# Kernel tuning notes

Hardware: AMD Instinct MI355X
Metric: run time of the kernel (lower is better)

The kernel has to match this reference:

```python
import jax, jax.numpy as jnp
import numpy as np

N_HEADS = 4
DIM_HEAD = 32
SCALE = DIM_HEAD ** -0.5
EPS = 1e-5


def setup_inputs() -> dict:
    key = jax.random.key(0)
    ks = jax.random.split(key, 5)
    b, dim, l, h, w = 8, 128, 32, 32, 32
    hidden = N_HEADS * DIM_HEAD  # 128
    return {
        "x": jax.random.normal(ks[0], (b, dim, l, h, w), dtype=jnp.float32),
        "w_qkv": jax.random.normal(ks[1], (3 * hidden, dim), dtype=jnp.float32) * 0.05,
        "w_out": jax.random.normal(ks[2], (dim, hidden), dtype=jnp.float32) * 0.05,
        "b_out": jax.random.normal(ks[3], (dim,), dtype=jnp.float32) * 0.05,
        "gn_gamma": jnp.ones((dim,), dtype=jnp.float32),
        "gn_beta": jnp.zeros((dim,), dtype=jnp.float32),
    }


def reference(x, w_qkv, w_out, b_out, gn_gamma, gn_beta):
    b, dim, l, h_sp, w_sp = x.shape
    n = l * h_sp * w_sp
    hidden = N_HEADS * DIM_HEAD
    xf = x.reshape(b, dim, n)  # flatten spatial -> tokens
    # 1x1 conv == channel matmul: [3*hidden, dim] x [b, dim, n]
    qkv = jnp.einsum('oc,bcn->bon', w_qkv, xf)
    qkv = qkv.reshape(b, 3, N_HEADS, DIM_HEAD, n)
    q, k, v = qkv[:, 0], qkv[:, 1], qkv[:, 2]  # each [b, H, d, n]
    q = jax.nn.softmax(q, axis=2) * SCALE      # softmax over feature dim d
    k = jax.nn.softmax(k, axis=-1)             # softmax over tokens n
    c = jnp.einsum('bhdn,bhen->bhde', k, v)    # [b, H, d, e] tiny context
    out = jnp.einsum('bhde,bhdn->bhen', c, q)  # [b, H, e, n]
    out = out.reshape(b, hidden, n)
    # to_out 1x1 conv + bias
    y = jnp.einsum('oc,bcn->bon', w_out, out) + b_out[None, :, None]
    # GroupNorm(1, dim): normalize over (C, spatial) per sample
    mean = jnp.mean(y, axis=(1, 2), keepdims=True)
    var = jnp.var(y, axis=(1, 2), keepdims=True)
    y = (y - mean) * jax.lax.rsqrt(var + EPS)
    y = y * gn_gamma[None, :, None] + gn_beta[None, :, None]
    return y.reshape(b, dim, l, h_sp, w_sp)
```

## Files before the change

### kernel.cpp

```cpp
#include <hip/hip_runtime.h>

#define BATCH 8
#define DIMC 128
#define NTOT 32768
#define HEADS 4
#define DHEAD 32
#define SCALE_Q 0.17677669529663687f
#define GRIDX 64
#define TILES 8

typedef _Float16 half8  __attribute__((ext_vector_type(8)));
typedef _Float16 half4v __attribute__((ext_vector_type(4)));
typedef float    f32x4  __attribute__((ext_vector_type(4)));

#define WS_WQKV 0
#define WS_S    98304
#define WS_Z    229376
#define WS_ST   233472
#define WS_GOFF 0
#define WS_NEED 299072


__global__ void k0_prep(const float* __restrict__ wqkv, char* __restrict__ ws) {
    int i = blockIdx.x * 256 + threadIdx.x;
    _Float16* Wb = (_Float16*)(ws + WS_WQKV);
    float* S  = (float*)(ws + WS_S);
    float* Z  = (float*)(ws + WS_Z);
    float* St = (float*)(ws + WS_ST);
    if (i < 49152) Wb[i] = (_Float16)wqkv[i];
    int j = i - 49152;
    if (j >= 0 && j < 32768) S[j] = 0.f;
    int k = j - 32768;
    if (k >= 0 && k < 1024) Z[k] = 0.f;
    int m = k - 1024;
    if (m >= 0 && m < 16) St[m] = 0.f;
}

__global__ __launch_bounds__(256, 1) void k1_kv(const float* __restrict__ x,
                                                const _Float16* __restrict__ Wb,
                                                float* __restrict__ S,
                                                float* __restrict__ Z,
                                                char* __restrict__ ybase) {
    __shared__ _Float16 Xb[64][136];
    __shared__ _Float16 KB[128][64];
    __shared__ _Float16 VB[128][64];
    __shared__ _Float16 EQT[64][136];
    const int t = threadIdx.x;
    const int lane = t & 63, w = t >> 6, g = lane >> 4, l15 = lane & 15;
    const int b = blockIdx.y;

    half8 wa[2][4];
    half8 af[4][4];
#pragma unroll
    for (int mi = 0; mi < 2; ++mi)
#pragma unroll
        for (int kc = 0; kc < 4; ++kc)
            wa[mi][kc] = *(const half8*)(Wb + (size_t)((w * 2 + mi) * 16 + l15) * 128 + kc * 32 + 8 * g);
#pragma unroll
    for (int mt = 0; mt < 4; ++mt)
#pragma unroll
        for (int kc = 0; kc < 4; ++kc)
            af[mt][kc] = *(const half8*)(Wb + (size_t)(128 + (w * 4 + mt) * 16 + l15) * 128 + kc * 32 + 8 * g);

    half8 vone;
#pragma unroll
    for (int i = 0; i < 8; ++i) vone[i] = (_Float16)1.0f;

    f32x4 sacc[2][2];
#pragma unroll
    for (int dm = 0; dm < 2; ++dm)
#pragma unroll
        for (int en = 0; en < 2; ++en) sacc[dm][en] = (f32x4){0.f, 0.f, 0.f, 0.f};
    f32x4 zacc[2];
    zacc[0] = (f32x4){0.f, 0.f, 0.f, 0.f};
    zacc[1] = (f32x4){0.f, 0.f, 0.f, 0.f};

    const int j4 = t & 15, c0 = t >> 4;
    const int sxw = (j4 & 7) << 3;

    float4 xr[8];
#pragma unroll
    for (int cc = 0; cc < 8; ++cc)
        xr[cc] = *(const float4*)(x + ((size_t)b * DIMC + c0 + 16 * cc) * NTOT + blockIdx.x * 64 + 4 * j4);
#pragma unroll
    for (int cc = 0; cc < 8; ++cc) {
        const int c = c0 + 16 * cc;
        Xb[4 * j4 + 0][c ^ sxw] = (_Float16)xr[cc].x;
        Xb[4 * j4 + 1][c ^ sxw] = (_Float16)xr[cc].y;
        Xb[4 * j4 + 2][c ^ sxw] = (_Float16)xr[cc].z;
        Xb[4 * j4 + 3][c ^ sxw] = (_Float16)xr[cc].w;
    }

    for (int it = 0; it < TILES; ++it) {
        const int j0 = (blockIdx.x + GRIDX * it) * 64;
        __syncthreads();
        half8 bf[4][4];
#pragma unroll
        for (int nt = 0; nt < 4; ++nt) {
            const int sb = ((4 * nt + (l15 >> 2)) & 7) << 3;
#pragma unroll
            for (int kc = 0; kc < 4; ++kc)
                bf[nt][kc] = *(const half8*)(&Xb[nt * 16 + l15][(kc * 32 + 8 * g) ^ sb]);
        }
        {
            f32x4 eacc[2][4];
#pragma unroll
            for (int mi = 0; mi < 2; ++mi)
#pragma unroll
                for (int nt = 0; nt < 4; ++nt) eacc[mi][nt] = (f32x4){0.f, 0.f, 0.f, 0.f};
#pragma unroll
            for (int mi = 0; mi < 2; ++mi)
#pragma unroll
                for (int kc = 0; kc < 4; ++kc)
#pragma unroll
                    for (int nt = 0; nt < 4; ++nt)
                        eacc[mi][nt] = __builtin_amdgcn_mfma_f32_16x16x32_f16(wa[mi][kc], bf[nt][kc], eacc[mi][nt], 0, 0, 0);
            float ps[4] = {0.f, 0.f, 0.f, 0.f};
#pragma unroll
            for (int mi = 0; mi < 2; ++mi)
#pragma unroll
                for (int nt = 0; nt < 4; ++nt)
#pragma unroll
                    for (int r = 0; r < 4; ++r) {
                        const float e = __expf(eacc[mi][nt][r]);
                        ps[nt] += e;
                        eacc[mi][nt][r] = e;
                    }
            float scn[4];
#pragma unroll
            for (int nt = 0; nt < 4; ++nt) {
                ps[nt] += __shfl_xor(ps[nt], 16);
                ps[nt] += __shfl_xor(ps[nt], 32);
                scn[nt] = SCALE_Q / ps[nt];
            }
#pragma unroll
            for (int mi = 0; mi < 2; ++mi)
#pragma unroll
                for (int nt = 0; nt < 4; ++nt) {
                    half4v p;
#pragma unroll
                    for (int r = 0; r < 4; ++r) p[r] = (_Float16)(eacc[mi][nt][r] * scn[nt]);
                    *(half4v*)(&EQT[nt * 16 + l15][(w * 2 + mi) * 16 + g * 4]) = p;
                }
        }
        if (it < TILES - 1) {
            const int j0n = (blockIdx.x + GRIDX * (it + 1)) * 64;
#pragma unroll
            for (int cc = 0; cc < 8; ++cc)
                xr[cc] = *(const float4*)(x + ((size_t)b * DIMC + c0 + 16 * cc) * NTOT + j0n + 4 * j4);
        }
#pragma unroll
        for (int mt = 0; mt < 4; ++mt) {
            f32x4 a0 = (f32x4){0.f,0.f,0.f,0.f}, a1 = a0, a2 = a0, a3 = a0;
#pragma unroll
            for (int kc = 0; kc < 4; ++kc) {
                a0 = __builtin_amdgcn_mfma_f32_16x16x32_f16(bf[0][kc], af[mt][kc], a0, 0, 0, 0);
                a1 = __builtin_amdgcn_mfma_f32_16x16x32_f16(bf[1][kc], af[mt][kc], a1, 0, 0, 0);
                a2 = __builtin_amdgcn_mfma_f32_16x16x32_f16(bf[2][kc], af[mt][kc], a2, 0, 0, 0);
                a3 = __builtin_amdgcn_mfma_f32_16x16x32_f16(bf[3][kc], af[mt][kc], a3, 0, 0, 0);
            }
            const int row16 = (w * 4 + mt) * 16;
            const int sk = ((mt * 4 + (l15 >> 2)) & 7) << 3;
            if (row16 < 128) {
#pragma unroll
                for (int jt = 0; jt < 4; ++jt) {
                    const f32x4 a = (jt == 0) ? a0 : (jt == 1) ? a1 : (jt == 2) ? a2 : a3;
                    half4v p;
#pragma unroll
                    for (int r = 0; r < 4; ++r) p[r] = (_Float16)__expf(a[r]);
                    *(half4v*)(&KB[row16 + l15][(jt * 16 + g * 4) ^ sk]) = p;
                }
            } else {
#pragma unroll
                for (int jt = 0; jt < 4; ++jt) {
                    const f32x4 a = (jt == 0) ? a0 : (jt == 1) ? a1 : (jt == 2) ? a2 : a3;
                    half4v p;
#pragma unroll
                    for (int r = 0; r < 4; ++r) p[r] = (_Float16)a[r];
                    *(half4v*)(&VB[row16 - 128 + l15][(jt * 16 + g * 4) ^ sk]) = p;
                }
            }
        }
        __syncthreads();
        if (it < TILES - 1) {
#pragma unroll
            for (int cc = 0; cc < 8; ++cc) {
                const int c = c0 + 16 * cc;
                Xb[4 * j4 + 0][c ^ sxw] = (_Float16)xr[cc].x;
                Xb[4 * j4 + 1][c ^ sxw] = (_Float16)xr[cc].y;
                Xb[4 * j4 + 2][c ^ sxw] = (_Float16)xr[cc].z;
                Xb[4 * j4 + 3][c ^ sxw] = (_Float16)xr[cc].w;
            }
        }
#pragma unroll
        for (int dm = 0; dm < 2; ++dm) {
            const int sr = ((4 * dm + (l15 >> 2)) & 7) << 3;
            half8 ka0 = *(const half8*)(&KB[w * 32 + dm * 16 + l15][(8 * g) ^ sr]);
            half8 ka1 = *(const half8*)(&KB[w * 32 + dm * 16 + l15][(32 + 8 * g) ^ sr]);
            zacc[dm] = __builtin_amdgcn_mfma_f32_16x16x32_f16(ka0, vone, zacc[dm], 0, 0, 0);
            zacc[dm] = __builtin_amdgcn_mfma_f32_16x16x32_f16(ka1, vone, zacc[dm], 0, 0, 0);
#pragma unroll
            for (int en = 0; en < 2; ++en) {
                const int se = ((4 * en + (l15 >> 2)) & 7) << 3;
                half8 vb0 = *(const half8*)(&VB[w * 32 + en * 16 + l15][(8 * g) ^ se]);
                half8 vb1 = *(const half8*)(&VB[w * 32 + en * 16 + l15][(32 + 8 * g) ^ se]);
                sacc[dm][en] = __builtin_amdgcn_mfma_f32_16x16x32_f16(ka0, vb0, sacc[dm][en], 0, 0, 0);
                sacc[dm][en] = __builtin_amdgcn_mfma_f32_16x16x32_f16(ka1, vb1, sacc[dm][en], 0, 0, 0);
            }
        }
        {
            char* tb = ybase + (size_t)(b * DIMC + (j0 >> 8)) * 131072 + (size_t)(j0 & 255) * 256;
#pragma unroll
            for (int p = 0; p < 4; ++p) {
                const int idx = p * 256 + t, jl = idx >> 4, d0 = (idx & 15) * 8;
                half8 v = *(const half8*)(&EQT[jl][d0]);
                *(half8*)(tb + (size_t)jl * 256 + d0 * 2) = v;
            }
        }
    }
    if (l15 == 0) {
#pragma unroll
        for (int dm = 0; dm < 2; ++dm)
#pragma unroll
            for (int r = 0; r < 4; ++r)
                atomicAdd(&Z[(b * HEADS + w) * DHEAD + dm * 16 + g * 4 + r], zacc[dm][r]);
    }
#pragma unroll
    for (int dm = 0; dm < 2; ++dm)
#pragma unroll
        for (int en = 0; en < 2; ++en)
#pragma unroll
            for (int r = 0; r < 4; ++r)
                atomicAdd(&S[((size_t)(b * HEADS + w) * DHEAD + dm * 16 + g * 4 + r) * DHEAD + en * 16 + l15],
                          sacc[dm][en][r]);
}

__global__ __launch_bounds__(256) void k2_g(const float* __restrict__ S, const float* __restrict__ Z,
                                            const float* __restrict__ wout, _Float16* __restrict__ G) {
    __shared__ float Sd[32][33];
    const int h = blockIdx.x, b = blockIdx.y;
    const int t = threadIdx.x;
    const float* Sb = S + (size_t)(b * HEADS + h) * 1024;
    const float* Zb = Z + (size_t)(b * HEADS + h) * 32;
    for (int i = t; i < 1024; i += 256) {
        int d = i >> 5;
        Sd[d][i & 31] = Sb[i] / Zb[d];
    }
    __syncthreads();
    const int o = t & 127, dh = (t >> 7) * 16;
    float wrow[32];
#pragma unroll
    for (int e = 0; e < 32; ++e) wrow[e] = wout[o * 128 + h * 32 + e];
    _Float16* Gb = G + (size_t)b * 16384;
#pragma unroll
    for (int dd = 0; dd < 16; ++dd) {
        const int d = dh + dd;
        float acc = 0.f;
#pragma unroll
        for (int e = 0; e < 32; ++e) acc = fmaf(wrow[e], Sd[d][e], acc);
        Gb[o * 128 + h * 32 + d] = (_Float16)acc;
    }
}

__global__ __launch_bounds__(256, 2) void k3_main(const _Float16* __restrict__ G,
                                                  const float* __restrict__ b_out,
                                                  char* __restrict__ ybase,
                                                  float* __restrict__ St) {
    __shared__ _Float16 EB[64][136];
    __shared__ float red[8];
    const int t = threadIdx.x;
    const int lane = t & 63, w = t >> 6, g = lane >> 4, l15 = lane & 15;
    const int b = blockIdx.y;

    half8 ga[2][4];
    float bo[2][4];
    const _Float16* Gb = G + (size_t)b * 16384;
#pragma unroll
    for (int mi = 0; mi < 2; ++mi) {
        const int o = (w * 2 + mi) * 16 + l15;
#pragma unroll
        for (int kc = 0; kc < 4; ++kc)
            ga[mi][kc] = *(const half8*)(Gb + (size_t)o * 128 + kc * 32 + 8 * g);
#pragma unroll
        for (int r = 0; r < 4; ++r) bo[mi][r] = b_out[(w * 2 + mi) * 16 + g * 4 + r];
    }

    float ssum = 0.f, ssq = 0.f;
    half8 er[4];

    {
        const int jb = blockIdx.x * 64;
        const char* tb = ybase + (size_t)(b * DIMC + (jb >> 8)) * 131072 + (size_t)(jb & 255) * 256;
#pragma unroll
        for (int p = 0; p < 4; ++p) {
            const int idx = p * 256 + t, jl = idx >> 4, d0 = (idx & 15) * 8;
            er[p] = *(const half8*)(tb + (size_t)jl * 256 + d0 * 2);
        }
#pragma unroll
        for (int p = 0; p < 4; ++p) {
            const int idx = p * 256 + t, jl = idx >> 4, d0 = (idx & 15) * 8;
            *(half8*)(&EB[jl][d0 ^ (((jl >> 2) & 7) << 3)]) = er[p];
        }
    }
    __syncthreads();

    for (int it = 0; it < TILES; ++it) {
        const int j0 = (blockIdx.x + GRIDX * it) * 64;
        if (it < TILES - 1) {
            const int jn = (blockIdx.x + GRIDX * (it + 1)) * 64;
            const char* tb = ybase + (size_t)(b * DIMC + (jn >> 8)) * 131072 + (size_t)(jn & 255) * 256;
#pragma unroll
            for (int p = 0; p < 4; ++p) {
                const int idx = p * 256 + t, jl = idx >> 4, d0 = (idx & 15) * 8;
                er[p] = *(const half8*)(tb + (size_t)jl * 256 + d0 * 2);
            }
        }
        {
            half8 bf[4][4];
#pragma unroll
            for (int nt = 0; nt < 4; ++nt) {
                const int sb = ((4 * nt + (l15 >> 2)) & 7) << 3;
#pragma unroll
                for (int kc = 0; kc < 4; ++kc)
                    bf[nt][kc] = *(const half8*)(&EB[nt * 16 + l15][(kc * 32 + 8 * g) ^ sb]);
            }
#pragma unroll
            for (int mi = 0; mi < 2; ++mi) {
                const int o0 = (w * 2 + mi) * 16 + g * 4;
                f32x4 acc[4];
#pragma unroll
                for (int nt = 0; nt < 4; ++nt) acc[nt] = (f32x4){0.f, 0.f, 0.f, 0.f};
#pragma unroll
                for (int kc = 0; kc < 4; ++kc)
#pragma unroll
                    for (int nt = 0; nt < 4; ++nt)
                        acc[nt] = __builtin_amdgcn_mfma_f32_16x16x32_f16(ga[mi][kc], bf[nt][kc], acc[nt], 0, 0, 0);
#pragma unroll
                for (int r = 0; r < 4; ++r) {
                    _Float16* yrow = (_Float16*)(ybase + (size_t)(b * DIMC + o0 + r) * 131072 + 65536);
#pragma unroll
                    for (int nt = 0; nt < 4; ++nt) {
                        const float yv = acc[nt][r] + bo[mi][r];
                        ssum += yv;
                        ssq += yv * yv;
                        yrow[j0 + nt * 16 + l15] = (_Float16)yv;
                    }
                }
            }
        }
        __syncthreads();
        if (it < TILES - 1) {
#pragma unroll
            for (int p = 0; p < 4; ++p) {
                const int idx = p * 256 + t, jl = idx >> 4, d0 = (idx & 15) * 8;
                *(half8*)(&EB[jl][d0 ^ (((jl >> 2) & 7) << 3)]) = er[p];
            }
        }
        __syncthreads();
    }
#pragma unroll
    for (int m = 32; m; m >>= 1) { ssum += __shfl_xor(ssum, m); ssq += __shfl_xor(ssq, m); }
    if (lane == 0) { red[w] = ssum; red[4 + w] = ssq; }
    __syncthreads();
    if (t == 0) {
        atomicAdd(&St[b * 2 + 0], red[0] + red[1] + red[2] + red[3]);
        atomicAdd(&St[b * 2 + 1], red[4] + red[5] + red[6] + red[7]);
    }
}

__global__ __launch_bounds__(256) void k4_norm(float* __restrict__ out, const float* __restrict__ St,
                                               const float* __restrict__ gamma,
                                               const float* __restrict__ beta) {
    const int o = blockIdx.x;
    const int b = blockIdx.y;
    const int t = threadIdx.x;
    const size_t row = (size_t)b * DIMC + o;
    const float n = (float)DIMC * (float)NTOT;
    const float mean = St[b * 2] / n;
    const float var = St[b * 2 + 1] / n - mean * mean;
    const float rs = rsqrtf(var + 1e-5f);
    const float ga = gamma[o] * rs;
    const float be = beta[o];
    const half8* yh = (const half8*)((const char*)out + row * 131072 + 65536);
    half8 hbuf[16];
#pragma unroll
    for (int i = 0; i < 16; ++i) hbuf[i] = yh[i * 256 + t];
    __syncthreads();
    float4* orow = (float4*)(out + row * NTOT);
#pragma unroll
    for (int i = 0; i < 16; ++i) {
        const int e4 = (i * 256 + t) * 2;
        float4 v0, v1;
        v0.x = ((float)hbuf[i][0] - mean) * ga + be;
        v0.y = ((float)hbuf[i][1] - mean) * ga + be;
        v0.z = ((float)hbuf[i][2] - mean) * ga + be;
        v0.w = ((float)hbuf[i][3] - mean) * ga + be;
        v1.x = ((float)hbuf[i][4] - mean) * ga + be;
        v1.y = ((float)hbuf[i][5] - mean) * ga + be;
        v1.z = ((float)hbuf[i][6] - mean) * ga + be;
        v1.w = ((float)hbuf[i][7] - mean) * ga + be;
        orow[e4] = v0;
        orow[e4 + 1] = v1;
    }
}

extern "C" void kernel_launch(void* const* d_in, const int* in_sizes, int n_in,
                              void* d_out, int out_size, void* d_ws, size_t ws_size,
                              hipStream_t stream) {
    const float* x     = (const float*)d_in[0];
    const float* wqkv  = (const float*)d_in[1];
    const float* wout  = (const float*)d_in[2];
    const float* b_out = (const float*)d_in[3];
    const float* gamma = (const float*)d_in[4];
    const float* beta  = (const float*)d_in[5];
    if (ws_size < WS_NEED) return;
    char* ws = (char*)d_ws;
    _Float16* Wb = (_Float16*)(ws + WS_WQKV);
    float* S  = (float*)(ws + WS_S);
    float* Z  = (float*)(ws + WS_Z);
    float* St = (float*)(ws + WS_ST);
    _Float16* G = (_Float16*)(ws + WS_GOFF);

    k0_prep<<<325, 256, 0, stream>>>(wqkv, ws);
    k1_kv<<<dim3(GRIDX, 8), 256, 0, stream>>>(x, Wb, S, Z, (char*)d_out);
    k2_g<<<dim3(HEADS, 8), 256, 0, stream>>>(S, Z, wout, G);
    k3_main<<<dim3(GRIDX, 8), 256, 0, stream>>>(G, b_out, (char*)d_out, St);
    k4_norm<<<dim3(128, 8), 256, 0, stream>>>((float*)d_out, St, gamma, beta);
}
```

Measured before the change: 156.9 us.

## Recompute q softmax in main kernel from x instead of storing it

The feature-dim q softmax moves out of the KV kernel and into the main output kernel, which now recomputes q from x on the fly. This removes the fp16 q write in the first pass and its read back in the main pass. In exchange, x is read twice in fp32 and the main kernel does extra MFMA and exp work. The main kernel's occupancy hint also drops from 2 to 1 block per CU. The G matrix now lives in spare space of the output buffer so that the fp16 W_qkv copy survives for the main kernel.

```diff
diff --git a/kernel.cpp b/kernel.cpp
--- a/kernel.cpp
+++ b/kernel.cpp
@@ -17,8 +17,7 @@
 #define WS_S    98304
 #define WS_Z    229376
 #define WS_ST   233472
-#define WS_GOFF 0
-#define WS_NEED 299072
+#define WS_NEED 233600
 
 
 __global__ void k0_prep(const float* __restrict__ wqkv, char* __restrict__ ws) {
@@ -39,23 +38,15 @@
 __global__ __launch_bounds__(256, 1) void k1_kv(const float* __restrict__ x,
                                                 const _Float16* __restrict__ Wb,
                                                 float* __restrict__ S,
-                                                float* __restrict__ Z,
-                                                char* __restrict__ ybase) {
+                                                float* __restrict__ Z) {
     __shared__ _Float16 Xb[64][136];
     __shared__ _Float16 KB[128][64];
     __shared__ _Float16 VB[128][64];
-    __shared__ _Float16 EQT[64][136];
     const int t = threadIdx.x;
     const int lane = t & 63, w = t >> 6, g = lane >> 4, l15 = lane & 15;
     const int b = blockIdx.y;
 
-    half8 wa[2][4];
     half8 af[4][4];
-#pragma unroll
-    for (int mi = 0; mi < 2; ++mi)
-#pragma unroll
-        for (int kc = 0; kc < 4; ++kc)
-            wa[mi][kc] = *(const half8*)(Wb + (size_t)((w * 2 + mi) * 16 + l15) * 128 + kc * 32 + 8 * g);
 #pragma unroll
     for (int mt = 0; mt < 4; ++mt)
 #pragma unroll
@@ -92,7 +83,6 @@
     }
 
     for (int it = 0; it < TILES; ++it) {
-        const int j0 = (blockIdx.x + GRIDX * it) * 64;
         __syncthreads();
         half8 bf[4][4];
 #pragma unroll
@@ -101,47 +91,6 @@
 #pragma unroll
             for (int kc = 0; kc < 4; ++kc)
                 bf[nt][kc] = *(const half8*)(&Xb[nt * 16 + l15][(kc * 32 + 8 * g) ^ sb]);
-        }
-        {
-            f32x4 eacc[2][4];
-#pragma unroll
-            for (int mi = 0; mi < 2; ++mi)
-#pragma unroll
-                for (int nt = 0; nt < 4; ++nt) eacc[mi][nt] = (f32x4){0.f, 0.f, 0.f, 0.f};
-#pragma unroll
-            for (int mi = 0; mi < 2; ++mi)
-#pragma unroll
-                for (int kc = 0; kc < 4; ++kc)
-#pragma unroll
-                    for (int nt = 0; nt < 4; ++nt)
-                        eacc[mi][nt] = __builtin_amdgcn_mfma_f32_16x16x32_f16(wa[mi][kc], bf[nt][kc], eacc[mi][nt], 0, 0, 0);
-            float ps[4] = {0.f, 0.f, 0.f, 0.f};
-#pragma unroll
-            for (int mi = 0; mi < 2; ++mi)
-#pragma unroll
-                for (int nt = 0; nt < 4; ++nt)
-#pragma unroll
-                    for (int r = 0; r < 4; ++r) {
-                        const float e = __expf(eacc[mi][nt][r]);
-                        ps[nt] += e;
-                        eacc[mi][nt][r] = e;
-                    }
-            float scn[4];
-#pragma unroll
-            for (int nt = 0; nt < 4; ++nt) {
-                ps[nt] += __shfl_xor(ps[nt], 16);
-                ps[nt] += __shfl_xor(ps[nt], 32);
-                scn[nt] = SCALE_Q / ps[nt];
-            }
-#pragma unroll
-            for (int mi = 0; mi < 2; ++mi)
-#pragma unroll
-                for (int nt = 0; nt < 4; ++nt) {
-                    half4v p;
-#pragma unroll
-                    for (int r = 0; r < 4; ++r) p[r] = (_Float16)(eacc[mi][nt][r] * scn[nt]);
-                    *(half4v*)(&EQT[nt * 16 + l15][(w * 2 + mi) * 16 + g * 4]) = p;
-                }
         }
         if (it < TILES - 1) {
             const int j0n = (blockIdx.x + GRIDX * (it + 1)) * 64;
@@ -208,15 +157,6 @@
                 sacc[dm][en] = __builtin_amdgcn_mfma_f32_16x16x32_f16(ka1, vb1, sacc[dm][en], 0, 0, 0);
             }
         }
-        {
-            char* tb = ybase + (size_t)(b * DIMC + (j0 >> 8)) * 131072 + (size_t)(j0 & 255) * 256;
-#pragma unroll
-            for (int p = 0; p < 4; ++p) {
-                const int idx = p * 256 + t, jl = idx >> 4, d0 = (idx & 15) * 8;
-                half8 v = *(const half8*)(&EQT[jl][d0]);
-                *(half8*)(tb + (size_t)jl * 256 + d0 * 2) = v;
-            }
-        }
     }
     if (l15 == 0) {
 #pragma unroll
@@ -236,7 +176,7 @@
 }
 
 __global__ __launch_bounds__(256) void k2_g(const float* __restrict__ S, const float* __restrict__ Z,
-                                            const float* __restrict__ wout, _Float16* __restrict__ G) {
+                                            const float* __restrict__ wout, char* __restrict__ ybase) {
     __shared__ float Sd[32][33];
     const int h = blockIdx.x, b = blockIdx.y;
     const int t = threadIdx.x;
@@ -251,7 +191,7 @@
     float wrow[32];
 #pragma unroll
     for (int e = 0; e < 32; ++e) wrow[e] = wout[o * 128 + h * 32 + e];
-    _Float16* Gb = G + (size_t)b * 16384;
+    _Float16* Gb = (_Float16*)(ybase + (size_t)(b * 16) * 131072);
 #pragma unroll
     for (int dd = 0; dd < 16; ++dd) {
         const int d = dh + dd;
@@ -262,58 +202,59 @@
     }
 }
 
-__global__ __launch_bounds__(256, 2) void k3_main(const _Float16* __restrict__ G,
+__global__ __launch_bounds__(256, 1) void k3_main(const float* __restrict__ x,
+                                                  const _Float16* __restrict__ Wb,
                                                   const float* __restrict__ b_out,
                                                   char* __restrict__ ybase,
                                                   float* __restrict__ St) {
-    __shared__ _Float16 EB[64][136];
+    __shared__ _Float16 Xb[64][136];
+    __shared__ _Float16 qT[64][136];
     __shared__ float red[8];
     const int t = threadIdx.x;
     const int lane = t & 63, w = t >> 6, g = lane >> 4, l15 = lane & 15;
     const int b = blockIdx.y;
-
+    const int j4 = t & 15, c0 = t >> 4;
+    const int sxw = (j4 & 7) << 3;
+
+    half8 wa[2][4];
     half8 ga[2][4];
     float bo[2][4];
-    const _Float16* Gb = G + (size_t)b * 16384;
+    const _Float16* Gb = (const _Float16*)(ybase + (size_t)(b * 16) * 131072);
 #pragma unroll
     for (int mi = 0; mi < 2; ++mi) {
         const int o = (w * 2 + mi) * 16 + l15;
 #pragma unroll
-        for (int kc = 0; kc < 4; ++kc)
+        for (int kc = 0; kc < 4; ++kc) {
+            wa[mi][kc] = *(const half8*)(Wb + (size_t)o * 128 + kc * 32 + 8 * g);
             ga[mi][kc] = *(const half8*)(Gb + (size_t)o * 128 + kc * 32 + 8 * g);
+        }
 #pragma unroll
         for (int r = 0; r < 4; ++r) bo[mi][r] = b_out[(w * 2 + mi) * 16 + g * 4 + r];
     }
 
     float ssum = 0.f, ssq = 0.f;
-    half8 er[4];
-
-    {
-        const int jb = blockIdx.x * 64;
-        const char* tb = ybase + (size_t)(b * DIMC + (jb >> 8)) * 131072 + (size_t)(jb & 255) * 256;
-#pragma unroll
-        for (int p = 0; p < 4; ++p) {
-            const int idx = p * 256 + t, jl = idx >> 4, d0 = (idx & 15) * 8;
-            er[p] = *(const half8*)(tb + (size_t)jl * 256 + d0 * 2);
-        }
-#pragma unroll
-        for (int p = 0; p < 4; ++p) {
-            const int idx = p * 256 + t, jl = idx >> 4, d0 = (idx & 15) * 8;
-            *(half8*)(&EB[jl][d0 ^ (((jl >> 2) & 7) << 3)]) = er[p];
-        }
+
+    float4 xr[8];
+#pragma unroll
+    for (int cc = 0; cc < 8; ++cc)
+        xr[cc] = *(const float4*)(x + ((size_t)b * DIMC + c0 + 16 * cc) * NTOT + blockIdx.x * 64 + 4 * j4);
+#pragma unroll
+    for (int cc = 0; cc < 8; ++cc) {
+        const int c = c0 + 16 * cc;
+        Xb[4 * j4 + 0][c ^ sxw] = (_Float16)xr[cc].x;
+        Xb[4 * j4 + 1][c ^ sxw] = (_Float16)xr[cc].y;
+        Xb[4 * j4 + 2][c ^ sxw] = (_Float16)xr[cc].z;
+        Xb[4 * j4 + 3][c ^ sxw] = (_Float16)xr[cc].w;
     }
     __syncthreads();
 
     for (int it = 0; it < TILES; ++it) {
         const int j0 = (blockIdx.x + GRIDX * it) * 64;
         if (it < TILES - 1) {
-            const int jn = (blockIdx.x + GRIDX * (it + 1)) * 64;
-            const char* tb = ybase + (size_t)(b * DIMC + (jn >> 8)) * 131072 + (size_t)(jn & 255) * 256;
-#pragma unroll
-            for (int p = 0; p < 4; ++p) {
-                const int idx = p * 256 + t, jl = idx >> 4, d0 = (idx & 15) * 8;
-                er[p] = *(const half8*)(tb + (size_t)jl * 256 + d0 * 2);
-            }
+            const int j0n = (blockIdx.x + GRIDX * (it + 1)) * 64;
+#pragma unroll
+            for (int cc = 0; cc < 8; ++cc)
+                xr[cc] = *(const float4*)(x + ((size_t)b * DIMC + c0 + 16 * cc) * NTOT + j0n + 4 * j4);
         }
         {
             half8 bf[4][4];
@@ -322,8 +263,66 @@
                 const int sb = ((4 * nt + (l15 >> 2)) & 7) << 3;
 #pragma unroll
                 for (int kc = 0; kc < 4; ++kc)
-                    bf[nt][kc] = *(const half8*)(&EB[nt * 16 + l15][(kc * 32 + 8 * g) ^ sb]);
-            }
+                    bf[nt][kc] = *(const half8*)(&Xb[nt * 16 + l15][(kc * 32 + 8 * g) ^ sb]);
+            }
+            f32x4 eacc[2][4];
+#pragma unroll
+            for (int mi = 0; mi < 2; ++mi)
+#pragma unroll
+                for (int nt = 0; nt < 4; ++nt) eacc[mi][nt] = (f32x4){0.f, 0.f, 0.f, 0.f};
+#pragma unroll
+            for (int mi = 0; mi < 2; ++mi)
+#pragma unroll
+                for (int kc = 0; kc < 4; ++kc)
+#pragma unroll
+                    for (int nt = 0; nt < 4; ++nt)
+                        eacc[mi][nt] = __builtin_amdgcn_mfma_f32_16x16x32_f16(wa[mi][kc], bf[nt][kc], eacc[mi][nt], 0, 0, 0);
+            float ps[4] = {0.f, 0.f, 0.f, 0.f};
+#pragma unroll
+            for (int mi = 0; mi < 2; ++mi)
+#pragma unroll
+                for (int nt = 0; nt < 4; ++nt)
+#pragma unroll
+                    for (int r = 0; r < 4; ++r) {
+                        const float e = __expf(eacc[mi][nt][r]);
+                        ps[nt] += e;
+                        eacc[mi][nt][r] = e;
+                    }
+            float scn[4];
+#pragma unroll
+            for (int nt = 0; nt < 4; ++nt) {
+                ps[nt] += __shfl_xor(ps[nt], 16);
+                ps[nt] += __shfl_xor(ps[nt], 32);
+                scn[nt] = SCALE_Q / ps[nt];
+            }
+#pragma unroll
+            for (int mi = 0; mi < 2; ++mi)
+#pragma unroll
+                for (int nt = 0; nt < 4; ++nt) {
+                    half4v p;
+#pragma unroll
+                    for (int r = 0; r < 4; ++r) p[r] = (_Float16)(eacc[mi][nt][r] * scn[nt]);
+                    *(half4v*)(&qT[nt * 16 + l15][((w * 2 + mi) * 16 + g * 4)]) = p;
+                }
+        }
+        __syncthreads();
+        if (it < TILES - 1) {
+#pragma unroll
+            for (int cc = 0; cc < 8; ++cc) {
+                const int c = c0 + 16 * cc;
+                Xb[4 * j4 + 0][c ^ sxw] = (_Float16)xr[cc].x;
+                Xb[4 * j4 + 1][c ^ sxw] = (_Float16)xr[cc].y;
+                Xb[4 * j4 + 2][c ^ sxw] = (_Float16)xr[cc].z;
+                Xb[4 * j4 + 3][c ^ sxw] = (_Float16)xr[cc].w;
+            }
+        }
+        {
+            half8 bf[4][4];
+#pragma unroll
+            for (int nt = 0; nt < 4; ++nt)
+#pragma unroll
+                for (int kc = 0; kc < 4; ++kc)
+                    bf[nt][kc] = *(const half8*)(&qT[nt * 16 + l15][kc * 32 + 8 * g]);
 #pragma unroll
             for (int mi = 0; mi < 2; ++mi) {
                 const int o0 = (w * 2 + mi) * 16 + g * 4;
@@ -346,14 +345,6 @@
                         yrow[j0 + nt * 16 + l15] = (_Float16)yv;
                     }
                 }
-            }
-        }
-        __syncthreads();
-        if (it < TILES - 1) {
-#pragma unroll
-            for (int p = 0; p < 4; ++p) {
-                const int idx = p * 256 + t, jl = idx >> 4, d0 = (idx & 15) * 8;
-                *(half8*)(&EB[jl][d0 ^ (((jl >> 2) & 7) << 3)]) = er[p];
             }
         }
         __syncthreads();
@@ -419,11 +410,10 @@
     float* S  = (float*)(ws + WS_S);
     float* Z  = (float*)(ws + WS_Z);
     float* St = (float*)(ws + WS_ST);
-    _Float16* G = (_Float16*)(ws + WS_GOFF);
 
     k0_prep<<<325, 256, 0, stream>>>(wqkv, ws);
-    k1_kv<<<dim3(GRIDX, 8), 256, 0, stream>>>(x, Wb, S, Z, (char*)d_out);
-    k2_g<<<dim3(HEADS, 8), 256, 0, stream>>>(S, Z, wout, G);
-    k3_main<<<dim3(GRIDX, 8), 256, 0, stream>>>(G, b_out, (char*)d_out, St);
+    k1_kv<<<dim3(GRIDX, 8), 256, 0, stream>>>(x, Wb, S, Z);
+    k2_g<<<dim3(HEADS, 8), 256, 0, stream>>>(S, Z, wout, (char*)d_out);
+    k3_main<<<dim3(GRIDX, 8), 256, 0, stream>>>(x, Wb, b_out, (char*)d_out, St);
     k4_norm<<<dim3(128, 8), 256, 0, stream>>>((float*)d_out, St, gamma, beta);
 }
```

New measurement: 165.9 us. 1.06x slower.
